# Kernel optimization log

Hardware: AMD Instinct MI355X
Metric: run time of the kernel (lower is better)

## Reference

```python
import jax, jax.numpy as jnp
import numpy as np

D = 768
H = 12
DH = D // H  # 64
LN_EPS = 1e-5


def layer_norm(x, gamma, beta):
    mu = jnp.mean(x, axis=-1, keepdims=True)
    var = jnp.var(x, axis=-1, keepdims=True)
    return (x - mu) * jax.lax.rsqrt(var + LN_EPS) * gamma + beta


def setup_inputs() -> dict:
    key = jax.random.key(0)
    ks = jax.random.split(key, 12)
    b, n1, n2 = 2, 4096, 4096
    s = 1.0 / np.sqrt(D)
    return {
        "input_cap": jax.random.normal(ks[0], (b, n1, D), jnp.float32),
        "output_cap": jax.random.normal(ks[1], (b, n2, D), jnp.float32),
        "Wq": jax.random.normal(ks[2], (D, D), jnp.float32) * s,
        "bq": jnp.zeros((D,), jnp.float32),
        "Wk": jax.random.normal(ks[3], (D, D), jnp.float32) * s,
        "bk": jnp.zeros((D,), jnp.float32),
        "Wv": jax.random.normal(ks[4], (D, D), jnp.float32) * s,
        "bv": jnp.zeros((D,), jnp.float32),
        "ln_g": jnp.ones((D,), jnp.float32),
        "ln_b": jnp.zeros((D,), jnp.float32),
        "Wp": jax.random.normal(ks[5], (D, D), jnp.float32) * s,
        "bp": jnp.zeros((D,), jnp.float32),
    }


def reference(input_cap, output_cap, Wq, bq, Wk, bk, Wv, bv, ln_g, ln_b, Wp, bp):
    b, n1, _ = input_cap.shape
    n2 = output_cap.shape[1]
    i = layer_norm(input_cap, ln_g, ln_b)   # shared LayerNorm, as in source
    o = layer_norm(output_cap, ln_g, ln_b)
    q = (o @ Wq.T + bq).reshape(b, n2, H, DH).transpose(0, 2, 1, 3)  # b h n2 dh
    k = (i @ Wk.T + bk).reshape(b, n1, H, DH).transpose(0, 2, 1, 3)  # b h n1 dh
    v = (i @ Wv.T + bv).reshape(b, n1, H, DH).transpose(0, 2, 1, 3)  # b h n1 dh
    scores = jnp.einsum("bhqd,bhkd->bhqk", q, k) / np.sqrt(DH)
    probs = jax.nn.softmax(scores, axis=-1)
    ctl = jnp.einsum("bhqk,bhkd->bhqd", probs, v)
    ctl = ctl.transpose(0, 2, 1, 3).reshape(b, n2, D)
    # DropPath is identity in eval mode
    return output_cap + ctl @ Wp.T + bp
```

## Files before the change

### kernel.cpp

```cpp
#include <hip/hip_runtime.h>


#define D 768
#define L2E 1.4426950408889634f
#define DEFER 11.5416f
#define NW 589824

typedef unsigned int u32;
typedef unsigned short u16;
typedef short bf16x8 __attribute__((ext_vector_type(8)));
typedef float f32x4 __attribute__((ext_vector_type(4)));
typedef float f32x16 __attribute__((ext_vector_type(16)));
typedef u16 u16x4 __attribute__((ext_vector_type(4)));
typedef u32 u32x4 __attribute__((ext_vector_type(4)));
typedef float f32x4v __attribute__((ext_vector_type(4)));

static __device__ __forceinline__ u16 f2bf(float f) {
  u32 b = __builtin_bit_cast(u32, f);
  b += 0x7FFFu + ((b >> 16) & 1u);
  return (u16)(b >> 16);
}

static __device__ __forceinline__ u32 cvtpk(float lo, float hi) {
  u32 r;
  asm("v_cvt_pk_bf16_f32 %0, %1, %2" : "=v"(r) : "v"(lo), "v"(hi));
  return r;
}

static __device__ __forceinline__ void plswap(u32& a, u32& b) {
  asm("v_permlane32_swap_b32 %0, %1" : "+v"(a), "+v"(b));
}

static __device__ __forceinline__ void gload_lds16(const u16* g, u16* l) {
  __builtin_amdgcn_global_load_lds(
      (const __attribute__((address_space(1))) unsigned int*)g,
      (__attribute__((address_space(3))) unsigned int*)l, 16, 0, 0);
}

#define MFMA16(a, b, c) __builtin_amdgcn_mfma_f32_16x16x32_bf16((a), (b), (c), 0, 0, 0)
#define MFMA32(a, b, c) __builtin_amdgcn_mfma_f32_32x32x16_bf16((a), (b), (c), 0, 0, 0)

__global__ __launch_bounds__(256) void ln_kernel(
    const float* __restrict__ icap, const float* __restrict__ ocap,
    const float* __restrict__ g, const float* __restrict__ be,
    u16* __restrict__ iln, u16* __restrict__ oln) {
  int r = blockIdx.x;
  const float* src; u16* dst; int rr;
  if (r < 8192) { src = icap; dst = iln; rr = r; }
  else          { src = ocap; dst = oln; rr = r - 8192; }
  const float* row = src + (size_t)rr * D;
  int t = threadIdx.x;
  float x0 = row[t], x1 = row[t + 256], x2 = row[t + 512];
  float s = x0 + x1 + x2;
  float q = x0 * x0 + x1 * x1 + x2 * x2;
#pragma unroll
  for (int off = 32; off > 0; off >>= 1) {
    s += __shfl_xor(s, off);
    q += __shfl_xor(q, off);
  }
  __shared__ float red[8];
  int w = t >> 6, lane = t & 63;
  if (lane == 0) { red[w] = s; red[4 + w] = q; }
  __syncthreads();
  s = red[0] + red[1] + red[2] + red[3];
  q = red[4] + red[5] + red[6] + red[7];
  float mu = s * (1.0f / 768.0f);
  float var = q * (1.0f / 768.0f) - mu * mu;
  float rs = rsqrtf(var + 1e-5f);
  u16* drow = dst + (size_t)rr * D;
  drow[t]       = f2bf((x0 - mu) * rs * g[t]       + be[t]);
  drow[t + 256] = f2bf((x1 - mu) * rs * g[t + 256] + be[t + 256]);
  drow[t + 512] = f2bf((x2 - mu) * rs * g[t + 512] + be[t + 512]);
}

__global__ __launch_bounds__(256) void wcast_kernel(
    const float* __restrict__ w0, const float* __restrict__ w1,
    const float* __restrict__ w2, const float* __restrict__ w3,
    u16* __restrict__ dst) {
  int wsel = blockIdx.y;
  const float* src = wsel == 0 ? w0 : wsel == 1 ? w1 : wsel == 2 ? w2 : w3;
  int i = (blockIdx.x * 256 + threadIdx.x) * 4;
  f32x4v v = *(const f32x4v*)(src + i);
  u16x4 o = { f2bf(v[0]), f2bf(v[1]), f2bf(v[2]), f2bf(v[3]) };
  *(u16x4*)(dst + (size_t)wsel * NW + i) = o;
}

static __device__ __forceinline__ void gemm_core_128(
    const u16* __restrict__ A, const u16* __restrict__ W,
    int mrow0, int nrow0, f32x4 (&acc)[4][4]) {
  __shared__ __align__(1024) u16 As[128 * 64];
  __shared__ __align__(1024) u16 Bs[128 * 64];
  const int tid = threadIdx.x;
  const int lane = tid & 63;
  const int w = tid >> 6;
  const int wr = (w >> 1) << 6, wc = (w & 1) << 6;
  const int l15 = lane & 15, lg = lane >> 4;
  const int lr = lane >> 3, lc = (lane & 7) << 3;

  for (int kt = 0; kt < D; kt += 64) {
#pragma unroll
    for (int j = 0; j < 4; ++j) {
      int c = w * 4 + j;
      const u16* ga = A + (size_t)(mrow0 + c * 8 + lr) * D + kt + lc;
      const u16* gb = W + (size_t)(nrow0 + c * 8 + lr) * D + kt + lc;
      gload_lds16(ga, &As[c * 512]);
      gload_lds16(gb, &Bs[c * 512]);
    }
    __syncthreads();
    bf16x8 af[4][2];
#pragma unroll
    for (int m = 0; m < 4; ++m) {
#pragma unroll
      for (int c = 0; c < 2; ++c)
        af[m][c] = *(const bf16x8*)&As[(wr + m * 16 + l15) * 64 + c * 32 + lg * 8];
    }
#pragma unroll
    for (int n = 0; n < 4; ++n) {
      bf16x8 b0 = *(const bf16x8*)&Bs[(wc + n * 16 + l15) * 64 + lg * 8];
      bf16x8 b1 = *(const bf16x8*)&Bs[(wc + n * 16 + l15) * 64 + 32 + lg * 8];
#pragma unroll
      for (int m = 0; m < 4; ++m) {
        acc[m][n] = MFMA16(af[m][0], b0, acc[m][n]);
        acc[m][n] = MFMA16(af[m][1], b1, acc[m][n]);
      }
    }
    __syncthreads();
  }
}

__global__ __launch_bounds__(256) void qkv_gemm(
    const u16* __restrict__ i_ln, const u16* __restrict__ o_ln,
    const u16* __restrict__ Wb,
    const float* __restrict__ bq, const float* __restrict__ bk,
    const float* __restrict__ bv,
    u16* __restrict__ qout, u16* __restrict__ kout, u16* __restrict__ vT) {
  const int mblk = blockIdx.x;
  const int ny = blockIdx.y;
  const int which = ny / 6;
  const int nb = ny % 6;
  const u16* A = (which == 0) ? o_ln : i_ln;
  const u16* W = Wb + (size_t)which * NW;
  const float* bias = (which == 0) ? bq : (which == 1) ? bk : bv;

  const f32x4 z = {0.f, 0.f, 0.f, 0.f};
  f32x4 acc[4][4];
#pragma unroll
  for (int m = 0; m < 4; ++m)
#pragma unroll
    for (int n = 0; n < 4; ++n) acc[m][n] = z;

  gemm_core_128(A, W, mblk * 128, nb * 128, acc);

  const int lane = threadIdx.x & 63, w = threadIdx.x >> 6;
  const int wr = (w >> 1) << 6, wc = (w & 1) << 6;
  const int l15 = lane & 15, lg = lane >> 4;
  const int m0 = mblk * 128 + wr;
  const int n0 = nb * 128 + wc;

  if (which == 2) {
#pragma unroll
    for (int m = 0; m < 4; ++m) {
#pragma unroll
      for (int n = 0; n < 4; ++n) {
        int gn = n0 + n * 16 + l15;
        float bi = bias[gn];
        int gm = m0 + m * 16 + lg * 4;
        int bidx = gm >> 12, seq = gm & 4095;
        u16x4 pk = { f2bf(acc[m][n][0] + bi), f2bf(acc[m][n][1] + bi),
                     f2bf(acc[m][n][2] + bi), f2bf(acc[m][n][3] + bi) };
        *(u16x4*)(vT + ((size_t)bidx * 768 + gn) * 4096 + seq) = pk;
      }
    }
  } else {
    u16* out = (which == 0) ? qout : kout;
    const float scale = (which == 0) ? 0.125f * L2E : 1.0f;
#pragma unroll
    for (int m = 0; m < 4; ++m) {
#pragma unroll
      for (int n = 0; n < 4; ++n) {
        int gn = n0 + n * 16 + l15;
        float bi = bias[gn];
#pragma unroll
        for (int r = 0; r < 4; ++r) {
          int gm = m0 + m * 16 + lg * 4 + r;
          out[(size_t)gm * D + gn] = f2bf((acc[m][n][r] + bi) * scale);
        }
      }
    }
  }
}

__global__ __launch_bounds__(256) void proj_gemm(
    const u16* __restrict__ ctl, const u16* __restrict__ Wpb,
    const float* __restrict__ bp, const float* __restrict__ res,
    float* __restrict__ out) {
  const int mblk = blockIdx.x;
  const int nb = blockIdx.y;
  const f32x4 z = {0.f, 0.f, 0.f, 0.f};
  f32x4 acc[4][4];
#pragma unroll
  for (int m = 0; m < 4; ++m)
#pragma unroll
    for (int n = 0; n < 4; ++n) acc[m][n] = z;

  gemm_core_128(ctl, Wpb, mblk * 128, nb * 128, acc);

  const int lane = threadIdx.x & 63, w = threadIdx.x >> 6;
  const int wr = (w >> 1) << 6, wc = (w & 1) << 6;
  const int l15 = lane & 15, lg = lane >> 4;
  const int m0 = mblk * 128 + wr;
  const int n0 = nb * 128 + wc;
#pragma unroll
  for (int m = 0; m < 4; ++m) {
#pragma unroll
    for (int n = 0; n < 4; ++n) {
      int gn = n0 + n * 16 + l15;
      float bi = bp[gn];
#pragma unroll
      for (int r = 0; r < 4; ++r) {
        int gm = m0 + m * 16 + lg * 4 + r;
        out[(size_t)gm * D + gn] = res[(size_t)gm * D + gn] + acc[m][n][r] + bi;
      }
    }
  }
}

__global__ __launch_bounds__(256, 3) void attn_kernel(
    const u16* __restrict__ q, const u16* __restrict__ k,
    const u16* __restrict__ vT, u16* __restrict__ ctl) {
  const int qb = blockIdx.x;
  const int bh = blockIdx.y;
  const int b = bh / 12, h = bh % 12;
  const int tid = threadIdx.x;
  const int lane = tid & 63, w = tid >> 6;
  const int l31 = lane & 31;
  const int hi = lane >> 5;
  const int swz = l31 & 7;

  __shared__ __align__(16) u16 Ks[64 * 64];
  __shared__ __align__(16) u16 Vs[64 * 64];

  const int qrow0 = qb * 128 + w * 32;
  const u16* qbase = q + (size_t)b * 4096 * D + h * 64;
  const u16* kbase = k + (size_t)b * 4096 * D + h * 64;
  const u16* vbase = vT + ((size_t)b * 768 + h * 64) * 4096;

  bf16x8 qf[4];
#pragma unroll
  for (int ks = 0; ks < 4; ++ks)
    qf[ks] = *(const bf16x8*)(qbase + (size_t)(qrow0 + l31) * D + ks * 16 + hi * 8);

  const bf16x8 ones = {0x3F80, 0x3F80, 0x3F80, 0x3F80, 0x3F80, 0x3F80, 0x3F80, 0x3F80};

  f32x16 acc[2], accl;
#pragma unroll
  for (int db = 0; db < 2; ++db)
#pragma unroll
    for (int r = 0; r < 16; ++r) acc[db][r] = 0.f;
#pragma unroll
  for (int r = 0; r < 16; ++r) accl[r] = 0.f;
  float m = -1e30f;

  const int r0 = tid >> 3, c0 = tid & 7;
  const int sc8 = (c0 ^ (r0 & 7)) << 3;
  uint4 vk0, vk1, vv0, vv1;
  vk0 = *(const uint4*)(kbase + (size_t)r0 * D + c0 * 8);
  vv0 = *(const uint4*)(vbase + (size_t)r0 * 4096 + c0 * 8);
  vk1 = *(const uint4*)(kbase + (size_t)(r0 + 32) * D + c0 * 8);
  vv1 = *(const uint4*)(vbase + (size_t)(r0 + 32) * 4096 + c0 * 8);

  for (int kv0 = 0; kv0 < 4096; kv0 += 64) {
    *(uint4*)&Ks[r0 * 64 + sc8] = vk0;
    *(uint4*)&Vs[r0 * 64 + sc8] = vv0;
    *(uint4*)&Ks[(r0 + 32) * 64 + sc8] = vk1;
    *(uint4*)&Vs[(r0 + 32) * 64 + sc8] = vv1;
    __syncthreads();

    if (kv0 + 64 < 4096) {
      int nx = kv0 + 64;
      vk0 = *(const uint4*)(kbase + (size_t)(nx + r0) * D + c0 * 8);
      vv0 = *(const uint4*)(vbase + (size_t)r0 * 4096 + nx + c0 * 8);
      vk1 = *(const uint4*)(kbase + (size_t)(nx + r0 + 32) * D + c0 * 8);
      vv1 = *(const uint4*)(vbase + (size_t)(r0 + 32) * 4096 + nx + c0 * 8);
    }

    f32x16 st[2];
    __builtin_amdgcn_s_setprio(1);
#pragma unroll
    for (int t = 0; t < 2; ++t) {
      f32x16 s;
#pragma unroll
      for (int r = 0; r < 16; ++r) s[r] = 0.f;
#pragma unroll
      for (int ks = 0; ks < 4; ++ks) {
        bf16x8 kf = *(const bf16x8*)&Ks[(t * 32 + l31) * 64 + ((2 * ks + hi) ^ swz) * 8];
        s = MFMA32(kf, qf[ks], s);
      }
      st[t] = s;
    }
    __builtin_amdgcn_s_setprio(0);

    float pmA = st[0][0], pmB = st[0][1], pmC = st[0][2], pmD = st[0][3];
#pragma unroll
    for (int r = 4; r < 16; r += 4) {
      pmA = fmaxf(pmA, st[0][r]);     pmB = fmaxf(pmB, st[0][r + 1]);
      pmC = fmaxf(pmC, st[0][r + 2]); pmD = fmaxf(pmD, st[0][r + 3]);
    }
#pragma unroll
    for (int r = 0; r < 16; r += 4) {
      pmA = fmaxf(pmA, st[1][r]);     pmB = fmaxf(pmB, st[1][r + 1]);
      pmC = fmaxf(pmC, st[1][r + 2]); pmD = fmaxf(pmD, st[1][r + 3]);
    }
    float pm = fmaxf(fmaxf(pmA, pmB), fmaxf(pmC, pmD));
    { u32 a = __builtin_bit_cast(u32, pm), bb = a;
      plswap(a, bb);
      float po = __builtin_bit_cast(float, hi ? a : bb);
      pm = fmaxf(pm, po); }

    if (pm > m + DEFER) {
      float es = __builtin_amdgcn_exp2f(m - pm);
      m = pm;
#pragma unroll
      for (int db = 0; db < 2; ++db)
#pragma unroll
        for (int r = 0; r < 16; ++r) acc[db][r] *= es;
#pragma unroll
      for (int r = 0; r < 16; ++r) accl[r] *= es;
    }

    bf16x8 pf[4];
#pragma unroll
    for (int t = 0; t < 2; ++t) {
      float p[16];
#pragma unroll
      for (int r = 0; r < 16; r += 4) {
        p[r]     = __builtin_amdgcn_exp2f(st[t][r] - m);
        p[r + 1] = __builtin_amdgcn_exp2f(st[t][r + 1] - m);
        p[r + 2] = __builtin_amdgcn_exp2f(st[t][r + 2] - m);
        p[r + 3] = __builtin_amdgcn_exp2f(st[t][r + 3] - m);
      }
      u32 a0 = cvtpk(p[0], p[1]),   a1 = cvtpk(p[2], p[3]);
      u32 b0 = cvtpk(p[4], p[5]),   b1 = cvtpk(p[6], p[7]);
      plswap(a0, b0); plswap(a1, b1);
      u32x4 w0 = {a0, a1, b0, b1};
      pf[2 * t] = __builtin_bit_cast(bf16x8, w0);
      u32 c0_ = cvtpk(p[8], p[9]),   c1 = cvtpk(p[10], p[11]);
      u32 d0 = cvtpk(p[12], p[13]), d1 = cvtpk(p[14], p[15]);
      plswap(c0_, d0); plswap(c1, d1);
      u32x4 w1 = {c0_, c1, d0, d1};
      pf[2 * t + 1] = __builtin_bit_cast(bf16x8, w1);
    }

    __builtin_amdgcn_s_setprio(1);
#pragma unroll
    for (int db = 0; db < 2; ++db)
#pragma unroll
      for (int ks = 0; ks < 4; ++ks) {
        bf16x8 vf = *(const bf16x8*)&Vs[(db * 32 + l31) * 64 + ((2 * ks + hi) ^ swz) * 8];
        acc[db] = MFMA32(vf, pf[ks], acc[db]);
      }
#pragma unroll
    for (int ks = 0; ks < 4; ++ks)
      accl = MFMA32(ones, pf[ks], accl);
    __builtin_amdgcn_s_setprio(0);
    __syncthreads();
  }

  float inv = 1.0f / accl[0];
  u16* cbase = ctl + ((size_t)b * 4096 + qrow0 + l31) * D + h * 64;
#pragma unroll
  for (int db = 0; db < 2; ++db)
#pragma unroll
    for (int rq = 0; rq < 4; ++rq) {
      u16x4 pkv = { f2bf(acc[db][rq * 4 + 0] * inv), f2bf(acc[db][rq * 4 + 1] * inv),
                    f2bf(acc[db][rq * 4 + 2] * inv), f2bf(acc[db][rq * 4 + 3] * inv) };
      *(u16x4*)(cbase + db * 32 + rq * 8 + hi * 4) = pkv;
    }
}

extern "C" void kernel_launch(void* const* d_in, const int* in_sizes, int n_in,
                              void* d_out, int out_size, void* d_ws, size_t ws_size,
                              hipStream_t stream) {
  const float* in_cap  = (const float*)d_in[0];
  const float* out_cap = (const float*)d_in[1];
  const float* Wq = (const float*)d_in[2];
  const float* bq = (const float*)d_in[3];
  const float* Wk = (const float*)d_in[4];
  const float* bk = (const float*)d_in[5];
  const float* Wv = (const float*)d_in[6];
  const float* bv = (const float*)d_in[7];
  const float* ln_g = (const float*)d_in[8];
  const float* ln_b = (const float*)d_in[9];
  const float* Wp = (const float*)d_in[10];
  const float* bp = (const float*)d_in[11];
  float* out = (float*)d_out;

  char* ws = (char*)d_ws;
  const size_t tsz = (size_t)8192 * D * 2;
  u16* i_ln = (u16*)(ws + 0 * tsz);
  u16* o_ln = (u16*)(ws + 1 * tsz);
  u16* qb_  = (u16*)(ws + 2 * tsz);
  u16* kb_  = (u16*)(ws + 3 * tsz);
  u16* vT   = (u16*)(ws + 4 * tsz);
  u16* ctl  = (u16*)(ws + 5 * tsz);
  u16* Wb   = (u16*)(ws + 6 * tsz);

  ln_kernel<<<dim3(16384), dim3(256), 0, stream>>>(in_cap, out_cap, ln_g, ln_b, i_ln, o_ln);
  wcast_kernel<<<dim3(576, 4), dim3(256), 0, stream>>>(Wq, Wk, Wv, Wp, Wb);
  qkv_gemm<<<dim3(64, 18), dim3(256), 0, stream>>>(i_ln, o_ln, Wb, bq, bk, bv, qb_, kb_, vT);
  attn_kernel<<<dim3(32, 24), dim3(256), 0, stream>>>(qb_, kb_, vT, ctl);
  proj_gemm<<<dim3(64, 6), dim3(256), 0, stream>>>(ctl, Wb + (size_t)3 * NW, bp, out_cap, out);
}
```

Baseline: 346.5 us.

## Split attention KV range in two and merge partials in a combine kernel

The attention kernel now splits the 4096-key range into two halves, doubling the grid, and writes unnormalized bf16 partial outputs plus the per-row max and sum to workspace. A new combine kernel rescales the two partials with exp2 weights, normalizes, and writes the context tensor in the original layout. Launch bounds are raised to 6 blocks per CU so the larger grid can be resident at once. In exchange this adds a kernel launch and extra global traffic for the partials. The tighter register budget may also cause spilling, and the partial outputs are rounded to bf16 before merging.

Measured after the change: 1.164 ms. +236.0%, slower.

```diff
diff --git a/kernel.cpp b/kernel.cpp
--- a/kernel.cpp
+++ b/kernel.cpp
@@ -19,6 +19,10 @@
   u32 b = __builtin_bit_cast(u32, f);
   b += 0x7FFFu + ((b >> 16) & 1u);
   return (u16)(b >> 16);
+}
+static __device__ __forceinline__ float bf2f(u16 h) {
+  u32 b = ((u32)h) << 16;
+  return __builtin_bit_cast(float, b);
 }
 
 static __device__ __forceinline__ u32 cvtpk(float lo, float hi) {
@@ -225,12 +229,17 @@
   }
 }
 
-__global__ __launch_bounds__(256, 3) void attn_kernel(
+__global__ __launch_bounds__(256, 6) void attn_kernel(
     const u16* __restrict__ q, const u16* __restrict__ k,
-    const u16* __restrict__ vT, u16* __restrict__ ctl) {
+    const u16* __restrict__ vT, u16* __restrict__ Opart,
+    float* __restrict__ mpart, float* __restrict__ lpart) {
   const int qb = blockIdx.x;
-  const int bh = blockIdx.y;
+  const int pair = blockIdx.y;
+  const int split = pair / 24;
+  const int bh = pair % 24;
   const int b = bh / 12, h = bh % 12;
+  const int s0 = split * 2048;
+
   const int tid = threadIdx.x;
   const int lane = tid & 63, w = tid >> 6;
   const int l31 = lane & 31;
@@ -264,19 +273,19 @@
   const int r0 = tid >> 3, c0 = tid & 7;
   const int sc8 = (c0 ^ (r0 & 7)) << 3;
   uint4 vk0, vk1, vv0, vv1;
-  vk0 = *(const uint4*)(kbase + (size_t)r0 * D + c0 * 8);
-  vv0 = *(const uint4*)(vbase + (size_t)r0 * 4096 + c0 * 8);
-  vk1 = *(const uint4*)(kbase + (size_t)(r0 + 32) * D + c0 * 8);
-  vv1 = *(const uint4*)(vbase + (size_t)(r0 + 32) * 4096 + c0 * 8);
-
-  for (int kv0 = 0; kv0 < 4096; kv0 += 64) {
+  vk0 = *(const uint4*)(kbase + (size_t)(s0 + r0) * D + c0 * 8);
+  vv0 = *(const uint4*)(vbase + (size_t)r0 * 4096 + s0 + c0 * 8);
+  vk1 = *(const uint4*)(kbase + (size_t)(s0 + r0 + 32) * D + c0 * 8);
+  vv1 = *(const uint4*)(vbase + (size_t)(r0 + 32) * 4096 + s0 + c0 * 8);
+
+  for (int kv0 = s0; kv0 < s0 + 2048; kv0 += 64) {
     *(uint4*)&Ks[r0 * 64 + sc8] = vk0;
     *(uint4*)&Vs[r0 * 64 + sc8] = vv0;
     *(uint4*)&Ks[(r0 + 32) * 64 + sc8] = vk1;
     *(uint4*)&Vs[(r0 + 32) * 64 + sc8] = vv1;
     __syncthreads();
 
-    if (kv0 + 64 < 4096) {
+    if (kv0 + 64 < s0 + 2048) {
       int nx = kv0 + 64;
       vk0 = *(const uint4*)(kbase + (size_t)(nx + r0) * D + c0 * 8);
       vv0 = *(const uint4*)(vbase + (size_t)r0 * 4096 + nx + c0 * 8);
@@ -366,16 +375,46 @@
     __syncthreads();
   }
 
-  float inv = 1.0f / accl[0];
-  u16* cbase = ctl + ((size_t)b * 4096 + qrow0 + l31) * D + h * 64;
+  u16* obase = Opart + ((size_t)pair * 4096 + qrow0 + l31) * 64;
 #pragma unroll
   for (int db = 0; db < 2; ++db)
 #pragma unroll
     for (int rq = 0; rq < 4; ++rq) {
-      u16x4 pkv = { f2bf(acc[db][rq * 4 + 0] * inv), f2bf(acc[db][rq * 4 + 1] * inv),
-                    f2bf(acc[db][rq * 4 + 2] * inv), f2bf(acc[db][rq * 4 + 3] * inv) };
-      *(u16x4*)(cbase + db * 32 + rq * 8 + hi * 4) = pkv;
-    }
+      u16x4 pkv = { f2bf(acc[db][rq * 4 + 0]), f2bf(acc[db][rq * 4 + 1]),
+                    f2bf(acc[db][rq * 4 + 2]), f2bf(acc[db][rq * 4 + 3]) };
+      *(u16x4*)(obase + db * 32 + rq * 8 + hi * 4) = pkv;
+    }
+  if (hi == 0) {
+    int idx = pair * 4096 + qrow0 + l31;
+    mpart[idx] = m;
+    lpart[idx] = accl[0];
+  }
+}
+
+__global__ __launch_bounds__(256) void combine_kernel(
+    const u16* __restrict__ Opart, const float* __restrict__ mpart,
+    const float* __restrict__ lpart, u16* __restrict__ ctl) {
+  int e8 = blockIdx.x * 256 + threadIdx.x;
+  int rowid = e8 >> 3;
+  int d0 = (e8 & 7) * 8;
+  float m0 = mpart[rowid], m1 = mpart[98304 + rowid];
+  float l0 = lpart[rowid], l1 = lpart[98304 + rowid];
+  float M = fmaxf(m0, m1);
+  float w0 = __builtin_amdgcn_exp2f(m0 - M);
+  float w1 = __builtin_amdgcn_exp2f(m1 - M);
+  float inv = 1.0f / (w0 * l0 + w1 * l1);
+  float a0 = w0 * inv, a1 = w1 * inv;
+  uint4 o0 = *(const uint4*)(Opart + (size_t)rowid * 64 + d0);
+  uint4 o1 = *(const uint4*)(Opart + ((size_t)98304 + rowid) * 64 + d0);
+  const u16* p0 = (const u16*)&o0;
+  const u16* p1 = (const u16*)&o1;
+  u16 ov[8];
+#pragma unroll
+  for (int j = 0; j < 8; ++j)
+    ov[j] = f2bf(a0 * bf2f(p0[j]) + a1 * bf2f(p1[j]));
+  int bh = rowid >> 12, qq = rowid & 4095;
+  int b = bh / 12, h = bh % 12;
+  *(uint4*)(ctl + ((size_t)b * 4096 + qq) * 768 + h * 64 + d0) = *(const uint4*)ov;
 }
 
 extern "C" void kernel_launch(void* const* d_in, const int* in_sizes, int n_in,
@@ -404,10 +443,14 @@
   u16* vT   = (u16*)(ws + 4 * tsz);
   u16* ctl  = (u16*)(ws + 5 * tsz);
   u16* Wb   = (u16*)(ws + 6 * tsz);
+  u16* Opart   = i_ln;
+  float* mpart = (float*)(ws + 6 * tsz);
+  float* lpart = (float*)(ws + 6 * tsz + (size_t)NW * 2);
 
   ln_kernel<<<dim3(16384), dim3(256), 0, stream>>>(in_cap, out_cap, ln_g, ln_b, i_ln, o_ln);
   wcast_kernel<<<dim3(576, 4), dim3(256), 0, stream>>>(Wq, Wk, Wv, Wp, Wb);
   qkv_gemm<<<dim3(64, 18), dim3(256), 0, stream>>>(i_ln, o_ln, Wb, bq, bk, bv, qb_, kb_, vT);
-  attn_kernel<<<dim3(32, 24), dim3(256), 0, stream>>>(qb_, kb_, vT, ctl);
+  attn_kernel<<<dim3(32, 48), dim3(256), 0, stream>>>(qb_, kb_, vT, Opart, mpart, lpart);
+  combine_kernel<<<dim3(3072), dim3(256), 0, stream>>>(Opart, mpart, lpart, ctl);
   proj_gemm<<<dim3(64, 6), dim3(256), 0, stream>>>(ctl, Wb + (size_t)3 * NW, bp, out_cap, out);
 }
```
